# Optimization experiments

Hardware: AMD Instinct MI355X
Metric: run time of the kernel (lower is better)

The kernel has to match this reference:

```python
import jax, jax.numpy as jnp
import numpy as np

SEM_DIM = 256
AC_DIM = 36
CODEBOOK_SIZE = 8192
FSQ_LEVELS = 21
COMMIT_COST = 0.25
HALF = (FSQ_LEVELS - 1) / 2.0  # 10.0
EPS = 0.001


def setup_inputs() -> dict:
    key = jax.random.key(0)
    k1, k2 = jax.random.split(key)
    z = jax.random.normal(k1, (8, SEM_DIM + AC_DIM, 4096), dtype=jnp.float32)
    lim = 1.0 / CODEBOOK_SIZE
    codebook = jax.random.uniform(k2, (CODEBOOK_SIZE, SEM_DIM), dtype=jnp.float32,
                                  minval=-lim, maxval=lim)
    return {"z": z, "codebook": codebook}


def _round_ste(x):
    return x + jax.lax.stop_gradient(jnp.round(x) - x)


def _vq(z_sem, codebook):
    # z_sem: (B, D, T), codebook: (K, D)
    B, D, T = z_sem.shape
    z_flat = jnp.transpose(z_sem, (0, 2, 1)).reshape(B * T, D)  # (N, D)
    # pairwise squared distances via matmul: ||z||^2 - 2 z.W^T + ||W||^2
    dists = (jnp.sum(z_flat * z_flat, axis=1, keepdims=True)
             - 2.0 * jnp.matmul(z_flat, codebook.T)
             + jnp.sum(codebook * codebook, axis=1)[None, :])  # (N, K)
    indices = jnp.argmin(dists, axis=1)  # (N,)
    z_q_flat = codebook[indices]  # (N, D) gather
    z_q = jnp.transpose(z_q_flat.reshape(B, T, D), (0, 2, 1))  # (B, D, T)
    codebook_loss = jnp.mean((z_q - jax.lax.stop_gradient(z_sem)) ** 2)
    commitment_loss = COMMIT_COST * jnp.mean((jax.lax.stop_gradient(z_q) - z_sem) ** 2)
    loss = codebook_loss + commitment_loss
    z_q_ste = z_sem + jax.lax.stop_gradient(z_q - z_sem)  # straight-through
    return z_q_ste, indices.reshape(B, T), loss


def _fsq(z_ac):
    z_b = jnp.tanh(z_ac) * (HALF + EPS)
    z_q = _round_ste(z_b)
    codes = jnp.clip((z_q + HALF).astype(jnp.int32), 0, FSQ_LEVELS - 1)
    return z_q, codes


def reference(z, codebook):
    z_sem = z[:, :SEM_DIM, :]
    z_ac = z[:, SEM_DIM:, :]
    z_sem_q, sem_indices, vq_loss = _vq(z_sem, codebook)
    z_ac_q, ac_codes = _fsq(z_ac)
    z_q = jnp.concatenate([z_sem_q, z_ac_q], axis=1)
    return (z_q, sem_indices, ac_codes, vq_loss, z_ac_q)
```

## Files before the change

kernel.cpp:

```cpp
#include <hip/hip_runtime.h>
#include <math.h>

#define BB 8
#define DSEM 256
#define DAC 36
#define DTOT 292
#define TT 4096
#define NCB 8192
#define NROWS (BB*TT)

static constexpr size_t O0 = 0;
static constexpr size_t O1 = 9568256;
static constexpr size_t O2 = 9601024;
static constexpr size_t O3 = 10780672;
static constexpr size_t O4 = 10780673;

static constexpr size_t WB_AH   = 0;
static constexpr size_t WB_BH   = 16777216;
static constexpr size_t WB_TMIN = 20971520;
static constexpr size_t WB_CBT  = 37748736;
static constexpr size_t WB_RN   = 46137344;
static constexpr size_t WB_CSQ  = 46268416;
static constexpr size_t WB_LOSS = 46301184;
static constexpr size_t WB_CNT  = 46301192;
static constexpr size_t WB_RN4  = 46301200;
static constexpr size_t WB_END  = 47349776;
static constexpr unsigned WL_CAP = 4194304;

typedef _Float16 f16x8 __attribute__((ext_vector_type(8)));
typedef __attribute__((ext_vector_type(4))) float f32x4;

__device__ __forceinline__ void gload_lds16(const void* g, void* lds) {
  __builtin_amdgcn_global_load_lds(
      (const __attribute__((address_space(1))) void*)g,
      (__attribute__((address_space(3))) void*)lds, 16, 0, 0);
}


__global__ __launch_bounds__(256) void k_fsq(const float* __restrict__ z,
                                             float* __restrict__ out) {
  int e = blockIdx.x * 256 + threadIdx.x;
  int b = e / (DAC * TT);
  int rem = e - b * (DAC * TT);
  int d = rem >> 12, t = rem & 4095;
  float zv = z[((size_t)(b * DTOT + DSEM + d) << 12) + t];
  float th = (float)tanh((double)zv);
  float zb = th * 10.001f;
  float zq = rintf(zb);
  int code = (int)(zq + 10.0f);
  code = code < 0 ? 0 : (code > 20 ? 20 : code);
  out[O0 + (((size_t)(b * DTOT + DSEM + d)) << 12) + t] = zq;
  out[O2 + e] = (float)code;
  out[O4 + e] = zq;
}


__global__ __launch_bounds__(256) void k_prepB2(const float* __restrict__ cb,
                                                _Float16* __restrict__ Bh,
                                                float* __restrict__ csq,
                                                float* __restrict__ cbT4,
                                                double* __restrict__ loss,
                                                unsigned* __restrict__ counters) {
  if (blockIdx.x == 0 && threadIdx.x == 0) {
    loss[0] = 0.0; counters[0] = 0u; counters[1] = 0u;
  }
  int e = blockIdx.x * 256 + threadIdx.x;
  float4 v = reinterpret_cast<const float4*>(cb)[e];
  union { _Float16 h[4]; short4 s4; } o;
  o.h[0] = (_Float16)(v.x * -32768.0f);
  o.h[1] = (_Float16)(v.y * -32768.0f);
  o.h[2] = (_Float16)(v.z * -32768.0f);
  o.h[3] = (_Float16)(v.w * -32768.0f);
  reinterpret_cast<short4*>(Bh)[e] = o.s4;
  float s = v.x * v.x + v.y * v.y + v.z * v.z + v.w * v.w;
  for (int off = 32; off; off >>= 1) s += __shfl_xor(s, off);
  if ((threadIdx.x & 63) == 0) csq[e >> 6] = s;
  int c = e & 31, r = e >> 5;
  int u = r >> 6, k4 = r & 63;
  int j = (u << 5) + c;
  float4 w = *reinterpret_cast<const float4*>(cb + (size_t)j * 256 + k4 * 4);
  reinterpret_cast<float4*>(cbT4)[e] = w;
}

__global__ __launch_bounds__(256) void k_prepA(const float* __restrict__ z,
                                               _Float16* __restrict__ Ah,
                                               float* __restrict__ outz,
                                               double* __restrict__ rn4) {
  __shared__ float tile[64][65];
  __shared__ double rpart[4][64];
  int bid = blockIdx.x;
  int tt = bid & 63, kt = (bid >> 6) & 3, b = bid >> 8;
  int k0 = kt * 64, t0 = tt * 64;
  int tid = threadIdx.x;
  int q = tid >> 6, t2r = tid & 63;
  double acc = 0.0;
  #pragma unroll
  for (int i = 0; i < 16; ++i) {
    int kk = i * 4 + q;
    float v = z[((size_t)(b * DTOT + k0 + kk) << 12) + t0 + t2r];
    tile[t2r][kk] = v;
    acc += (double)v * (double)v;
  }
  rpart[q][t2r] = acc;
  __syncthreads();
  float* zTb = outz + (size_t)b * (DTOT * TT);
  #pragma unroll
  for (int i = 0; i < 4; ++i) {
    int flat = i * 256 + tid;
    int t2 = flat >> 4, k4g = (flat & 15) << 2;
    float f0 = tile[t2][k4g + 0], f1 = tile[t2][k4g + 1];
    float f2 = tile[t2][k4g + 2], f3 = tile[t2][k4g + 3];
    union { _Float16 h[4]; short4 s; } hh;
    hh.h[0] = (_Float16)f0; hh.h[1] = (_Float16)f1;
    hh.h[2] = (_Float16)f2; hh.h[3] = (_Float16)f3;
    *reinterpret_cast<short4*>(
        Ah + (size_t)(b * 4096 + t0 + t2) * 256 + k0 + k4g) = hh.s;
    float4 ff;
    ff.x = f0; ff.y = f1; ff.z = f2; ff.w = f3;
    *reinterpret_cast<float4*>(
        zTb + (size_t)(t0 + t2) * 256 + k0 + k4g) = ff;
  }
  if (tid < 64) {
    double s = ((rpart[0][tid] + rpart[1][tid]) + rpart[2][tid]) + rpart[3][tid];
    rn4[(size_t)kt * NROWS + (b << 12) + t0 + tid] = s;
  }
}

__global__ __launch_bounds__(256) void k_gemm(const _Float16* __restrict__ A,
                                              const _Float16* __restrict__ B,
                                              const float* __restrict__ csq,
                                              _Float16* __restrict__ tmin) {
  __shared__ char smraw[128 * 68 * 4];
  _Float16* As = (_Float16*)smraw;
  _Float16* Bs = (_Float16*)(smraw + 16384);
  float* red = (float*)smraw;
  const float SCALE = 6.103515625e-05f;

  int bid = blockIdx.x;
  int wg = (bid & 7) * 2048 + (bid >> 3);
  int mtile = wg >> 6, ntile = wg & 63;
  int rbase = mtile << 7, cbase = ntile << 7;
  int tid = threadIdx.x, lane = tid & 63, wid = tid >> 6;
  int wm = wid >> 1, wn = wid & 1;
  int l15 = lane & 15, l4 = lane >> 4;
  int sw = l15 & 7;

  f32x4 acc[4][4];
  #pragma unroll
  for (int mi = 0; mi < 4; ++mi)
    #pragma unroll
    for (int ni = 0; ni < 4; ++ni) acc[mi][ni] = (f32x4){0.f, 0.f, 0.f, 0.f};

  for (int kt = 0; kt < 4; ++kt) {
    int kb = kt << 6;
    __syncthreads();
    #pragma unroll
    for (int i = 0; i < 4; ++i) {
      int flat = (wid * 4 + i) * 64 + lane;
      int row = flat >> 3;
      int csrc = (flat & 7) ^ (row & 7);
      gload_lds16(A + (size_t)(rbase + row) * 256 + kb + (csrc << 3),
                  (char*)As + flat * 16);
      gload_lds16(B + (size_t)(cbase + row) * 256 + kb + (csrc << 3),
                  (char*)Bs + flat * 16);
    }
    __syncthreads();
    #pragma unroll
    for (int ks = 0; ks < 2; ++ks) {
      int off = ((((ks << 2) + l4) ^ sw) << 3);
      f16x8 af[4], bv[4];
      #pragma unroll
      for (int mi = 0; mi < 4; ++mi)
        af[mi] = *(const f16x8*)(As + ((wm * 64 + mi * 16 + l15) << 6) + off);
      #pragma unroll
      for (int ni = 0; ni < 4; ++ni)
        bv[ni] = *(const f16x8*)(Bs + ((wn * 64 + ni * 16 + l15) << 6) + off);
      #pragma unroll
      for (int mi = 0; mi < 4; ++mi)
        #pragma unroll
        for (int ni = 0; ni < 4; ++ni)
          acc[mi][ni] = __builtin_amdgcn_mfma_f32_16x16x32_f16(af[mi], bv[ni], acc[mi][ni], 0, 0, 0);
    }
  }

  float csv[4];
  #pragma unroll
  for (int ni = 0; ni < 4; ++ni) csv[ni] = csq[cbase + wn * 64 + ni * 16 + l15];

  __syncthreads();
  #pragma unroll
  for (int mi = 0; mi < 4; ++mi) {
    #pragma unroll
    for (int r = 0; r < 4; ++r) {
      int row = wm * 64 + mi * 16 + l4 * 4 + r;
      float v0 = fminf(fmaf(acc[mi][0][r], SCALE, csv[0]),
                       fmaf(acc[mi][1][r], SCALE, csv[1]));
      float v1 = fminf(fmaf(acc[mi][2][r], SCALE, csv[2]),
                       fmaf(acc[mi][3][r], SCALE, csv[3]));
      red[row * 68 + (wn * 2 + 0) * 16 + l15] = v0;
      red[row * 68 + (wn * 2 + 1) * 16 + l15] = v1;
    }
  }
  __syncthreads();
  if (tid < 128) {
    int row = tid;
    const float* rp = red + row * 68;
    union { _Float16 h[4]; short4 s; } uu;
    #pragma unroll
    for (int q = 0; q < 4; ++q) {
      float m = rp[q * 16];
      #pragma unroll
      for (int x = 1; x < 16; ++x) m = fminf(m, rp[q * 16 + x]);
      uu.h[q] = (_Float16)m;
    }
    *reinterpret_cast<short4*>(tmin + (size_t)(rbase + row) * 256 + ntile * 4) = uu.s;
  }
}

__global__ __launch_bounds__(256) void k_cand(const _Float16* __restrict__ tmin,
                                              const double* __restrict__ rn4,
                                              float* __restrict__ rn,
                                              unsigned* __restrict__ wl,
                                              unsigned* __restrict__ counter,
                                              unsigned long long* __restrict__ result) {
  __shared__ unsigned long long smask[16][4];
  __shared__ unsigned scnt[16];
  __shared__ unsigned soff[16];
  int tid = threadIdx.x;
  int wv = tid >> 6, lane = tid & 63;
  int row0 = blockIdx.x << 4;

  for (int rr = wv; rr < 16; rr += 4) {
    int row = row0 + rr;
    const _Float16* tp = tmin + (size_t)row * 256;
    float v[4];
    #pragma unroll
    for (int i = 0; i < 4; ++i) v[i] = (float)tp[i * 64 + lane];
    float g = fminf(fminf(v[0], v[1]), fminf(v[2], v[3]));
    #pragma unroll
    for (int off = 32; off; off >>= 1) g = fminf(g, __shfl_xor(g, off));
    float thr = g + 1.5e-4f;
    if (lane == 0) {
      result[row] = 0xFFFFFFFFFFFFFFFFULL;
      double s = ((rn4[row] + rn4[NROWS + row]) + rn4[2 * NROWS + row]) +
                 rn4[3 * NROWS + row];
      rn[row] = (float)s;
    }
    unsigned cnt = 0;
    #pragma unroll
    for (int i = 0; i < 4; ++i) {
      unsigned long long mask = __ballot(v[i] <= thr);
      if (lane == 0) smask[rr][i] = mask;
      cnt += (unsigned)__popcll(mask);
    }
    if (lane == 0) scnt[rr] = cnt;
  }
  __syncthreads();
  if (tid == 0) {
    unsigned tot = 0;
    #pragma unroll
    for (int r = 0; r < 16; ++r) { soff[r] = tot; tot += scnt[r]; }
    unsigned base = atomicAdd(counter, tot);
    #pragma unroll
    for (int r = 0; r < 16; ++r) soff[r] += base;
  }
  __syncthreads();
  for (int rr = wv; rr < 16; rr += 4) {
    int row = row0 + rr;
    unsigned off = soff[rr];
    unsigned acc = 0;
    #pragma unroll
    for (int i = 0; i < 4; ++i) {
      unsigned long long mask = smask[rr][i];
      bool c = (mask >> lane) & 1ULL;
      if (c) {
        unsigned rank = acc + (unsigned)__popcll(mask & ((1ULL << lane) - 1ULL));
        unsigned idx = off + rank;
        if (idx < WL_CAP) wl[idx] = ((unsigned)row << 8) | (unsigned)(i * 64 + lane);
      }
      acc += (unsigned)__popcll(mask);
    }
  }
}

__global__ __launch_bounds__(256) void k_scan(const float* __restrict__ zT,
                                              const float* __restrict__ cbT4,
                                              const float* __restrict__ csq,
                                              const float* __restrict__ rn,
                                              const unsigned* __restrict__ wl,
                                              const unsigned* __restrict__ counter,
                                              unsigned long long* __restrict__ result) {
  unsigned total = *counter;
  if (total > WL_CAP) total = WL_CAP;
  int tid = threadIdx.x;
  unsigned stride = gridDim.x * 8u;
  int gw = blockIdx.x * 4 + (tid >> 6);
  int half = (tid >> 5) & 1, l32 = tid & 31;
  for (unsigned it = (unsigned)(gw * 2 + half); it < total; it += stride) {
    unsigned e = wl[it];
    int row = (int)(e >> 8), u = (int)(e & 255u);
    int j = (u << 5) + l32;
    int b = row >> 12, t = row & 4095;
    const float4* zp = reinterpret_cast<const float4*>(
        zT + (size_t)b * (DTOT * TT) + (size_t)t * 256);
    const float4* cp = reinterpret_cast<const float4*>(cbT4) + ((u * 64) * 32 + l32);
    float an = rn[row], cq = csq[j];
    float m0 = 0.f, m1 = 0.f, m2 = 0.f, m3 = 0.f;
    #pragma unroll 8
    for (int k4 = 0; k4 < 64; ++k4) {
      float4 cv = cp[k4 * 32];
      float4 zv = zp[k4];
      m0 = fmaf(zv.x, cv.x, m0);
      m1 = fmaf(zv.y, cv.y, m1);
      m2 = fmaf(zv.z, cv.z, m2);
      m3 = fmaf(zv.w, cv.w, m3);
    }
    float m = (m0 + m1) + (m2 + m3);
    float d = (an - 2.f * m) + cq;
    unsigned long long pk =
        (((unsigned long long)__float_as_uint(d)) << 32) | (unsigned)j;
    #pragma unroll
    for (int off = 16; off; off >>= 1) {
      unsigned long long o = __shfl_xor(pk, off);
      if (o < pk) pk = o;
    }
    if (l32 == 0) atomicMin(result + row, pk);
  }
}

__global__ __launch_bounds__(256) void k_out(const float* __restrict__ z,
                                             const float* __restrict__ cb,
                                             const unsigned long long* __restrict__ result,
                                             float* __restrict__ out0,
                                             float* __restrict__ out1,
                                             double* __restrict__ loss,
                                             unsigned* __restrict__ done,
                                             float* __restrict__ out3) {
  __shared__ float zs[32][257];
  __shared__ float hsum[8];
  int bid = blockIdx.x;
  int tt = bid & 127, b = bid >> 7;
  int t0 = tt * 32;
  int tid = threadIdx.x;

  #pragma unroll
  for (int i = 0; i < 8; ++i) {
    int flat = i * 256 + tid;
    int d = flat >> 3, t4 = (flat & 7) * 4;
    float4 v = *reinterpret_cast<const float4*>(
        z + ((size_t)(b * DTOT + d) << 12) + t0 + t4);
    zs[t4 + 0][d] = v.x; zs[t4 + 1][d] = v.y;
    zs[t4 + 2][d] = v.z; zs[t4 + 3][d] = v.w;
  }
  __syncthreads();

  int hw = tid >> 5, l32 = tid & 31;
  float lsum = 0.f;
  #pragma unroll
  for (int p = 0; p < 4; ++p) {
    int t2 = p * 8 + hw;
    int row = (b << 12) + t0 + t2;
    unsigned j = (unsigned)(result[row] & 0xFFFFFFFFULL);
    if (l32 == 0) out1[row] = (float)j;
    const float4* cp = reinterpret_cast<const float4*>(cb + (size_t)j * 256);
    float4 c0 = cp[l32 * 2], c1 = cp[l32 * 2 + 1];
    int d0 = l32 * 8;
    float cs = 0.f, df;
    df = c0.x - zs[t2][d0 + 0]; cs = fmaf(df, df, cs); zs[t2][d0 + 0] = c0.x;
    df = c0.y - zs[t2][d0 + 1]; cs = fmaf(df, df, cs); zs[t2][d0 + 1] = c0.y;
    df = c0.z - zs[t2][d0 + 2]; cs = fmaf(df, df, cs); zs[t2][d0 + 2] = c0.z;
    df = c0.w - zs[t2][d0 + 3]; cs = fmaf(df, df, cs); zs[t2][d0 + 3] = c0.w;
    df = c1.x - zs[t2][d0 + 4]; cs = fmaf(df, df, cs); zs[t2][d0 + 4] = c1.x;
    df = c1.y - zs[t2][d0 + 5]; cs = fmaf(df, df, cs); zs[t2][d0 + 5] = c1.y;
    df = c1.z - zs[t2][d0 + 6]; cs = fmaf(df, df, cs); zs[t2][d0 + 6] = c1.z;
    df = c1.w - zs[t2][d0 + 7]; cs = fmaf(df, df, cs); zs[t2][d0 + 7] = c1.w;
    lsum += cs;
  }
  #pragma unroll
  for (int off = 16; off; off >>= 1) lsum += __shfl_xor(lsum, off);
  if (l32 == 0) hsum[hw] = lsum;
  __syncthreads();

  #pragma unroll
  for (int i = 0; i < 8; ++i) {
    int flat = i * 256 + tid;
    int d = flat >> 3, t4 = (flat & 7) * 4;
    float4 v;
    v.x = zs[t4 + 0][d]; v.y = zs[t4 + 1][d];
    v.z = zs[t4 + 2][d]; v.w = zs[t4 + 3][d];
    *reinterpret_cast<float4*>(
        out0 + ((size_t)(b * DTOT + d) << 12) + t0 + t4) = v;
  }

  if (tid == 0) {
    float tot = ((hsum[0] + hsum[1]) + (hsum[2] + hsum[3])) +
                ((hsum[4] + hsum[5]) + (hsum[6] + hsum[7]));
    atomicAdd(loss, (double)tot);
    __threadfence();
    unsigned old = atomicAdd(done, 1u);
    if (old == 1023u) {
      double total = atomicAdd(loss, 0.0);
      out3[0] = (float)(1.25 * total / 8388608.0);
    }
  }
}


__global__ __launch_bounds__(256) void k_csq(const float* __restrict__ cb,
                                             float* __restrict__ csq,
                                             double* __restrict__ loss,
                                             unsigned* __restrict__ counter) {
  if (blockIdx.x == 0 && threadIdx.x == 0) { loss[0] = 0.0; counter[0] = 0u; }
  int w = (blockIdx.x << 2) + (threadIdx.x >> 6);
  int lane = threadIdx.x & 63;
  float4 v = *reinterpret_cast<const float4*>(cb + (size_t)w * DSEM + lane * 4);
  float s = v.x * v.x + v.y * v.y + v.z * v.z + v.w * v.w;
  for (int off = 32; off; off >>= 1) s += __shfl_xor(s, off);
  if (lane == 0) csq[w] = s;
}

__global__ __launch_bounds__(256) void k_rn(const float* __restrict__ z,
                                            float* __restrict__ rn) {
  int r = blockIdx.x * 256 + threadIdx.x;
  int b = r >> 12, t = r & 4095;
  const float* p = z + ((size_t)(b * DTOT) << 12) + t;
  double acc = 0.0;
  #pragma unroll 8
  for (int d = 0; d < DSEM; ++d) {
    float v = p[(size_t)d << 12];
    acc += (double)v * (double)v;
  }
  rn[r] = (float)acc;
}

__global__ void k_fin(const double* __restrict__ loss, float* __restrict__ out3) {
  out3[0] = (float)(1.25 * loss[0] / 8388608.0);
}

__global__ __launch_bounds__(256) void k_vq(const float* __restrict__ z,
                                            const float* __restrict__ cb,
                                            const float* __restrict__ csq,
                                            const float* __restrict__ rn,
                                            float* __restrict__ pmin,
                                            int* __restrict__ pidx) {
  __shared__ float As[32][132];
  __shared__ float Bs[32][132];
  const int tid = threadIdx.x;
  const int tx = tid & 15, ty = tid >> 4;
  const int mb = blockIdx.x >> 2, s = blockIdx.x & 3;
  const int r0 = mb << 7;
  const int b = r0 >> 12, t0 = r0 & 4095;
  const int nbase = s * 2048;

  int mrow[8], jcol[8];
  #pragma unroll
  for (int i = 0; i < 4; ++i) {
    mrow[i] = ty * 4 + i;  mrow[i + 4] = 64 + ty * 4 + i;
    jcol[i] = tx * 4 + i;  jcol[i + 4] = 64 + tx * 4 + i;
  }
  float an[8];
  #pragma unroll
  for (int i = 0; i < 8; ++i) an[i] = rn[r0 + mrow[i]];

  float rmin[8]; int ridx[8];
  #pragma unroll
  for (int i = 0; i < 8; ++i) { rmin[i] = 3.402823466e38f; ridx[i] = 0; }

  for (int nc = 0; nc < 16; ++nc) {
    const int n0 = nbase + nc * 128;
    float acc[8][8];
    #pragma unroll
    for (int i = 0; i < 8; ++i)
      #pragma unroll
      for (int j = 0; j < 8; ++j) acc[i][j] = 0.f;

    for (int kc = 0; kc < 8; ++kc) {
      const int kb = kc << 5;
      __syncthreads();
      #pragma unroll
      for (int i = 0; i < 4; ++i) {
        int flat = i * 256 + tid;
        int k = flat >> 5, m4 = (flat & 31) << 2;
        float4 vv = *reinterpret_cast<const float4*>(
            z + ((size_t)(b * DTOT + kb + k) << 12) + t0 + m4);
        *reinterpret_cast<float4*>(&As[k][m4]) = vv;
      }
      #pragma unroll
      for (int i = 0; i < 4; ++i) {
        int flat = i * 256 + tid;
        int j = flat >> 3, k4 = (flat & 7) << 2;
        float4 vv = *reinterpret_cast<const float4*>(
            cb + ((size_t)(n0 + j) << 8) + kb + k4);
        Bs[k4 + 0][j] = vv.x; Bs[k4 + 1][j] = vv.y;
        Bs[k4 + 2][j] = vv.z; Bs[k4 + 3][j] = vv.w;
      }
      __syncthreads();
      #pragma unroll 8
      for (int k = 0; k < 32; ++k) {
        float a[8], bv[8];
        *reinterpret_cast<float4*>(&a[0]) = *reinterpret_cast<const float4*>(&As[k][ty * 4]);
        *reinterpret_cast<float4*>(&a[4]) = *reinterpret_cast<const float4*>(&As[k][64 + ty * 4]);
        *reinterpret_cast<float4*>(&bv[0]) = *reinterpret_cast<const float4*>(&Bs[k][tx * 4]);
        *reinterpret_cast<float4*>(&bv[4]) = *reinterpret_cast<const float4*>(&Bs[k][64 + tx * 4]);
        #pragma unroll
        for (int i = 0; i < 8; ++i)
          #pragma unroll
          for (int j = 0; j < 8; ++j) acc[i][j] = fmaf(a[i], bv[j], acc[i][j]);
      }
    }
    float cs[8];
    #pragma unroll
    for (int j = 0; j < 8; ++j) cs[j] = csq[n0 + jcol[j]];
    #pragma unroll
    for (int i = 0; i < 8; ++i) {
      #pragma unroll
      for (int j = 0; j < 8; ++j) {
        float d = (an[i] - 2.f * acc[i][j]) + cs[j];
        int jg = n0 + jcol[j];
        if (d < rmin[i] || (d == rmin[i] && jg < ridx[i])) { rmin[i] = d; ridx[i] = jg; }
      }
    }
  }
  __syncthreads();
  float* redf = &As[0][0];
  int* redi = reinterpret_cast<int*>(&Bs[0][0]);
  #pragma unroll
  for (int i = 0; i < 8; ++i) {
    redf[mrow[i] * 16 + tx] = rmin[i];
    redi[mrow[i] * 16 + tx] = ridx[i];
  }
  __syncthreads();
  if (tid < 128) {
    int row = tid;
    float bestv = redf[row * 16]; int bi = redi[row * 16];
    #pragma unroll
    for (int x = 1; x < 16; ++x) {
      float m = redf[row * 16 + x]; int ii = redi[row * 16 + x];
      if (m < bestv || (m == bestv && ii < bi)) { bestv = m; bi = ii; }
    }
    pmin[(size_t)(r0 + row) * 4 + s] = bestv;
    pidx[(size_t)(r0 + row) * 4 + s] = bi;
  }
}

__global__ __launch_bounds__(256) void k_comb(const float* __restrict__ pmin,
                                              const int* __restrict__ pidx,
                                              int* __restrict__ widx,
                                              float* __restrict__ out1) {
  int r = blockIdx.x * 256 + threadIdx.x;
  float best = pmin[r * 4]; int bi = pidx[r * 4];
  #pragma unroll
  for (int s2 = 1; s2 < 4; ++s2) {
    float m = pmin[r * 4 + s2]; int ii = pidx[r * 4 + s2];
    if (m < best || (m == best && ii < bi)) { best = m; bi = ii; }
  }
  widx[r] = bi;
  out1[r] = (float)bi;
}

__global__ __launch_bounds__(256) void k_loss_fb(const float* __restrict__ z,
                                                 const float* __restrict__ cb,
                                                 const int* __restrict__ idx,
                                                 float* __restrict__ out0,
                                                 double* __restrict__ loss) {
  float s = 0.f;
  for (int e = blockIdx.x * 256 + threadIdx.x; e < BB * DSEM * TT; e += 2048 * 256) {
    int b = e >> 20;
    int rem = e & 1048575;
    int d = rem >> 12, t = rem & 4095;
    int r = (b << 12) + t;
    int j = idx[r];
    float c = cb[(size_t)j * DSEM + d];
    size_t zi = ((size_t)(b * DTOT + d) << 12) + t;
    float zv = z[zi];
    out0[zi] = c;
    float df = c - zv;
    s += df * df;
  }
  for (int off = 32; off; off >>= 1) s += __shfl_xor(s, off);
  __shared__ float ws4[4];
  int lane = threadIdx.x & 63, w = threadIdx.x >> 6;
  if (lane == 0) ws4[w] = s;
  __syncthreads();
  if (threadIdx.x == 0) {
    float tot = ws4[0] + ws4[1] + ws4[2] + ws4[3];
    atomicAdd(loss, (double)tot);
  }
}


extern "C" void kernel_launch(void* const* d_in, const int* in_sizes, int n_in,
                              void* d_out, int out_size, void* d_ws, size_t ws_size,
                              hipStream_t stream) {
  const float* z  = (const float*)d_in[0];
  const float* cb = (const float*)d_in[1];
  float* out = (float*)d_out;

  if (ws_size >= WB_END) {
    char* wsb = (char*)d_ws;
    _Float16* Ah   = (_Float16*)(wsb + WB_AH);
    _Float16* Bh   = (_Float16*)(wsb + WB_BH);
    _Float16* tmin = (_Float16*)(wsb + WB_TMIN);
    float*    cbT4 = (float*)(wsb + WB_CBT);
    float*    rn   = (float*)(wsb + WB_RN);
    float*    csq  = (float*)(wsb + WB_CSQ);
    double*   loss = (double*)(wsb + WB_LOSS);
    unsigned* counters = (unsigned*)(wsb + WB_CNT);
    double*   rn4  = (double*)(wsb + WB_RN4);
    unsigned* wl = (unsigned*)(wsb + WB_AH);
    unsigned long long* result = (unsigned long long*)(wsb + WB_BH);
    float* zT = out + O0;

    k_prepB2<<<2048, 256, 0, stream>>>(cb, Bh, csq, cbT4, loss, counters);
    k_fsq<<<(BB * DAC * TT) / 256, 256, 0, stream>>>(z, out);
    k_prepA<<<2048, 256, 0, stream>>>(z, Ah, zT, rn4);
    k_gemm<<<16384, 256, 0, stream>>>(Ah, Bh, csq, tmin);
    k_cand<<<NROWS / 16, 256, 0, stream>>>(tmin, rn4, rn, wl, counters, result);
    k_scan<<<4096, 256, 0, stream>>>(zT, cbT4, csq, rn, wl, counters, result);
    k_out<<<1024, 256, 0, stream>>>(z, cb, result, out + O0, out + O1, loss,
                                    counters + 1, out + O3);
  } else {
    float* wsf = (float*)d_ws;
    float* csq  = wsf;
    float* rn   = wsf + 8192;
    float* pmin = wsf + 40960;
    int*   pidx = (int*)(wsf + 172032);
    int*   widx = (int*)(wsf + 303104);
    double* loss = (double*)(wsf + 335872);
    unsigned* counter = (unsigned*)(wsf + 335876);

    k_csq<<<NCB / 4, 256, 0, stream>>>(cb, csq, loss, counter);
    k_rn<<<NROWS / 256, 256, 0, stream>>>(z, rn);
    k_fsq<<<(BB * DAC * TT) / 256, 256, 0, stream>>>(z, out);
    k_vq<<<(NROWS / 128) * 4, 256, 0, stream>>>(z, cb, csq, rn, pmin, pidx);
    k_comb<<<NROWS / 256, 256, 0, stream>>>(pmin, pidx, widx, out + O1);
    k_loss_fb<<<2048, 256, 0, stream>>>(z, cb, widx, out + O0, loss);
    k_fin<<<1, 1, 0, stream>>>(loss, out + O3);
  }
}
```

Before: 366.5 us.

## Replace candidate worklist with codebook-tile-major scan using LDS-resident codebook slices

The per-tile minimum matrix is now stored transposed (tile-major), and k_cand only computes a per-row threshold instead of building a compacted worklist with atomics. k_scan is reorganised so each block owns one 32-entry codebook tile, loads that slice into shared memory once, and sweeps a quarter of the rows, ballotting candidates against the threshold and refining them with exact fp32 dot products. This removes the global atomic worklist, its capacity limit, and the repeated global reads of codebook slices. In exchange, work is less balanced: blocks whose tiles have many candidates serialise them, and every block reads the full tmin column for its rows. The tmin stores in the GEMM epilogue also become scattered 2-byte writes.

New measurement: 375.7 us. 1.03x slower.

```diff
diff --git a/kernel.cpp b/kernel.cpp
--- a/kernel.cpp
+++ b/kernel.cpp
@@ -24,8 +24,8 @@
 static constexpr size_t WB_LOSS = 46301184;
 static constexpr size_t WB_CNT  = 46301192;
 static constexpr size_t WB_RN4  = 46301200;
-static constexpr size_t WB_END  = 47349776;
-static constexpr unsigned WL_CAP = 4194304;
+static constexpr size_t WB_THR  = 47349776;
+static constexpr size_t WB_END  = 47480848;
 
 typedef _Float16 f16x8 __attribute__((ext_vector_type(8)));
 typedef __attribute__((ext_vector_type(4))) float f32x4;
@@ -129,7 +129,7 @@
 __global__ __launch_bounds__(256) void k_gemm(const _Float16* __restrict__ A,
                                               const _Float16* __restrict__ B,
                                               const float* __restrict__ csq,
-                                              _Float16* __restrict__ tmin) {
+                                              _Float16* __restrict__ tminT) {
   __shared__ char smraw[128 * 68 * 4];
   _Float16* As = (_Float16*)smraw;
   _Float16* Bs = (_Float16*)(smraw + 16384);
@@ -205,126 +205,98 @@
   if (tid < 128) {
     int row = tid;
     const float* rp = red + row * 68;
-    union { _Float16 h[4]; short4 s; } uu;
     #pragma unroll
     for (int q = 0; q < 4; ++q) {
       float m = rp[q * 16];
       #pragma unroll
       for (int x = 1; x < 16; ++x) m = fminf(m, rp[q * 16 + x]);
-      uu.h[q] = (_Float16)m;
-    }
-    *reinterpret_cast<short4*>(tmin + (size_t)(rbase + row) * 256 + ntile * 4) = uu.s;
-  }
-}
-
-__global__ __launch_bounds__(256) void k_cand(const _Float16* __restrict__ tmin,
+      tminT[(size_t)(ntile * 4 + q) * NROWS + rbase + row] = (_Float16)m;
+    }
+  }
+}
+
+__global__ __launch_bounds__(256) void k_cand(const _Float16* __restrict__ tminT,
                                               const double* __restrict__ rn4,
                                               float* __restrict__ rn,
-                                              unsigned* __restrict__ wl,
-                                              unsigned* __restrict__ counter,
+                                              float* __restrict__ rowthr,
                                               unsigned long long* __restrict__ result) {
-  __shared__ unsigned long long smask[16][4];
-  __shared__ unsigned scnt[16];
-  __shared__ unsigned soff[16];
+  __shared__ float pmin[4][64];
   int tid = threadIdx.x;
-  int wv = tid >> 6, lane = tid & 63;
-  int row0 = blockIdx.x << 4;
-
-  for (int rr = wv; rr < 16; rr += 4) {
-    int row = row0 + rr;
-    const _Float16* tp = tmin + (size_t)row * 256;
-    float v[4];
-    #pragma unroll
-    for (int i = 0; i < 4; ++i) v[i] = (float)tp[i * 64 + lane];
-    float g = fminf(fminf(v[0], v[1]), fminf(v[2], v[3]));
-    #pragma unroll
-    for (int off = 32; off; off >>= 1) g = fminf(g, __shfl_xor(g, off));
-    float thr = g + 1.5e-4f;
-    if (lane == 0) {
-      result[row] = 0xFFFFFFFFFFFFFFFFULL;
-      double s = ((rn4[row] + rn4[NROWS + row]) + rn4[2 * NROWS + row]) +
-                 rn4[3 * NROWS + row];
-      rn[row] = (float)s;
-    }
-    unsigned cnt = 0;
-    #pragma unroll
-    for (int i = 0; i < 4; ++i) {
-      unsigned long long mask = __ballot(v[i] <= thr);
-      if (lane == 0) smask[rr][i] = mask;
-      cnt += (unsigned)__popcll(mask);
-    }
-    if (lane == 0) scnt[rr] = cnt;
-  }
-  __syncthreads();
-  if (tid == 0) {
-    unsigned tot = 0;
-    #pragma unroll
-    for (int r = 0; r < 16; ++r) { soff[r] = tot; tot += scnt[r]; }
-    unsigned base = atomicAdd(counter, tot);
-    #pragma unroll
-    for (int r = 0; r < 16; ++r) soff[r] += base;
-  }
-  __syncthreads();
-  for (int rr = wv; rr < 16; rr += 4) {
-    int row = row0 + rr;
-    unsigned off = soff[rr];
-    unsigned acc = 0;
-    #pragma unroll
-    for (int i = 0; i < 4; ++i) {
-      unsigned long long mask = smask[rr][i];
-      bool c = (mask >> lane) & 1ULL;
-      if (c) {
-        unsigned rank = acc + (unsigned)__popcll(mask & ((1ULL << lane) - 1ULL));
-        unsigned idx = off + rank;
-        if (idx < WL_CAP) wl[idx] = ((unsigned)row << 8) | (unsigned)(i * 64 + lane);
-      }
-      acc += (unsigned)__popcll(mask);
-    }
+  int w = tid >> 6, lane = tid & 63;
+  int row = (blockIdx.x << 6) + lane;
+  float g = 3.402823466e38f;
+  for (int ug = 0; ug < 64; ++ug) {
+    int u = w * 64 + ug;
+    g = fminf(g, (float)tminT[(size_t)u * NROWS + row]);
+  }
+  pmin[w][lane] = g;
+  __syncthreads();
+  if (w == 0) {
+    float gg = fminf(fminf(pmin[0][lane], pmin[1][lane]),
+                     fminf(pmin[2][lane], pmin[3][lane]));
+    rowthr[row] = gg + 1.5e-4f;
+    result[row] = 0xFFFFFFFFFFFFFFFFULL;
+    double s = ((rn4[row] + rn4[NROWS + row]) + rn4[2 * NROWS + row]) +
+               rn4[3 * NROWS + row];
+    rn[row] = (float)s;
   }
 }
 
 __global__ __launch_bounds__(256) void k_scan(const float* __restrict__ zT,
-                                              const float* __restrict__ cbT4,
+                                              const float4* __restrict__ cbT4f4,
                                               const float* __restrict__ csq,
                                               const float* __restrict__ rn,
-                                              const unsigned* __restrict__ wl,
-                                              const unsigned* __restrict__ counter,
+                                              const _Float16* __restrict__ tminT,
+                                              const float* __restrict__ rowthr,
                                               unsigned long long* __restrict__ result) {
-  unsigned total = *counter;
-  if (total > WL_CAP) total = WL_CAP;
+  __shared__ float4 cbl[2048];
+  int bid = blockIdx.x;
+  int u = bid >> 2, rc = bid & 3;
   int tid = threadIdx.x;
-  unsigned stride = gridDim.x * 8u;
-  int gw = blockIdx.x * 4 + (tid >> 6);
-  int half = (tid >> 5) & 1, l32 = tid & 31;
-  for (unsigned it = (unsigned)(gw * 2 + half); it < total; it += stride) {
-    unsigned e = wl[it];
-    int row = (int)(e >> 8), u = (int)(e & 255u);
-    int j = (u << 5) + l32;
-    int b = row >> 12, t = row & 4095;
-    const float4* zp = reinterpret_cast<const float4*>(
-        zT + (size_t)b * (DTOT * TT) + (size_t)t * 256);
-    const float4* cp = reinterpret_cast<const float4*>(cbT4) + ((u * 64) * 32 + l32);
-    float an = rn[row], cq = csq[j];
-    float m0 = 0.f, m1 = 0.f, m2 = 0.f, m3 = 0.f;
-    #pragma unroll 8
-    for (int k4 = 0; k4 < 64; ++k4) {
-      float4 cv = cp[k4 * 32];
-      float4 zv = zp[k4];
-      m0 = fmaf(zv.x, cv.x, m0);
-      m1 = fmaf(zv.y, cv.y, m1);
-      m2 = fmaf(zv.z, cv.z, m2);
-      m3 = fmaf(zv.w, cv.w, m3);
-    }
-    float m = (m0 + m1) + (m2 + m3);
-    float d = (an - 2.f * m) + cq;
-    unsigned long long pk =
-        (((unsigned long long)__float_as_uint(d)) << 32) | (unsigned)j;
-    #pragma unroll
-    for (int off = 16; off; off >>= 1) {
-      unsigned long long o = __shfl_xor(pk, off);
-      if (o < pk) pk = o;
-    }
-    if (l32 == 0) atomicMin(result + row, pk);
+  #pragma unroll
+  for (int i = 0; i < 8; ++i)
+    cbl[i * 256 + tid] = cbT4f4[(size_t)u * 2048 + i * 256 + tid];
+  __syncthreads();
+  int w = tid >> 6, lane = tid & 63, l32 = tid & 31;
+  int j = (u << 5) + l32;
+  float cq = csq[j];
+  int rbase0 = rc * 8192 + w * 2048;
+  for (int chunk = 0; chunk < 32; ++chunk) {
+    int rowb = rbase0 + chunk * 64;
+    float v = (float)tminT[(size_t)u * NROWS + rowb + lane];
+    float thr = rowthr[rowb + lane];
+    unsigned long long mask = __ballot(v <= thr);
+    while (mask) {
+      int sl0 = __builtin_ctzll(mask); mask &= mask - 1;
+      int sl1 = sl0;
+      if (mask) { sl1 = __builtin_ctzll(mask); mask &= mask - 1; }
+      int sl = (lane < 32) ? sl0 : sl1;
+      int crow = rowb + sl;
+      int b = crow >> 12, t = crow & 4095;
+      const float4* zp = reinterpret_cast<const float4*>(
+          zT + (size_t)b * (DTOT * TT) + (size_t)t * 256);
+      float an = rn[crow];
+      float m0 = 0.f, m1 = 0.f, m2 = 0.f, m3 = 0.f;
+      #pragma unroll 8
+      for (int k4 = 0; k4 < 64; ++k4) {
+        float4 cv = cbl[k4 * 32 + l32];
+        float4 zv = zp[k4];
+        m0 = fmaf(zv.x, cv.x, m0);
+        m1 = fmaf(zv.y, cv.y, m1);
+        m2 = fmaf(zv.z, cv.z, m2);
+        m3 = fmaf(zv.w, cv.w, m3);
+      }
+      float m = (m0 + m1) + (m2 + m3);
+      float d = (an - 2.f * m) + cq;
+      unsigned long long pk =
+          (((unsigned long long)__float_as_uint(d)) << 32) | (unsigned)j;
+      #pragma unroll
+      for (int off = 16; off; off >>= 1) {
+        unsigned long long o = __shfl_xor(pk, off);
+        if (o < pk) pk = o;
+      }
+      if (l32 == 0) atomicMin(result + crow, pk);
+    }
   }
 }
 
@@ -598,25 +570,26 @@
 
   if (ws_size >= WB_END) {
     char* wsb = (char*)d_ws;
-    _Float16* Ah   = (_Float16*)(wsb + WB_AH);
-    _Float16* Bh   = (_Float16*)(wsb + WB_BH);
-    _Float16* tmin = (_Float16*)(wsb + WB_TMIN);
-    float*    cbT4 = (float*)(wsb + WB_CBT);
-    float*    rn   = (float*)(wsb + WB_RN);
-    float*    csq  = (float*)(wsb + WB_CSQ);
-    double*   loss = (double*)(wsb + WB_LOSS);
+    _Float16* Ah    = (_Float16*)(wsb + WB_AH);
+    _Float16* Bh    = (_Float16*)(wsb + WB_BH);
+    _Float16* tminT = (_Float16*)(wsb + WB_TMIN);
+    float*    cbT4  = (float*)(wsb + WB_CBT);
+    float*    rn    = (float*)(wsb + WB_RN);
+    float*    csq   = (float*)(wsb + WB_CSQ);
+    double*   loss  = (double*)(wsb + WB_LOSS);
     unsigned* counters = (unsigned*)(wsb + WB_CNT);
-    double*   rn4  = (double*)(wsb + WB_RN4);
-    unsigned* wl = (unsigned*)(wsb + WB_AH);
+    double*   rn4   = (double*)(wsb + WB_RN4);
+    float*    rowthr = (float*)(wsb + WB_THR);
     unsigned long long* result = (unsigned long long*)(wsb + WB_BH);
     float* zT = out + O0;
 
     k_prepB2<<<2048, 256, 0, stream>>>(cb, Bh, csq, cbT4, loss, counters);
     k_fsq<<<(BB * DAC * TT) / 256, 256, 0, stream>>>(z, out);
     k_prepA<<<2048, 256, 0, stream>>>(z, Ah, zT, rn4);
-    k_gemm<<<16384, 256, 0, stream>>>(Ah, Bh, csq, tmin);
-    k_cand<<<NROWS / 16, 256, 0, stream>>>(tmin, rn4, rn, wl, counters, result);
-    k_scan<<<4096, 256, 0, stream>>>(zT, cbT4, csq, rn, wl, counters, result);
+    k_gemm<<<16384, 256, 0, stream>>>(Ah, Bh, csq, tminT);
+    k_cand<<<NROWS / 64, 256, 0, stream>>>(tminT, rn4, rn, rowthr, result);
+    k_scan<<<1024, 256, 0, stream>>>(zT, (const float4*)cbT4, csq, rn, tminT,
+                                     rowthr, result);
     k_out<<<1024, 256, 0, stream>>>(z, cb, result, out + O0, out + O1, loss,
                                     counters + 1, out + O3);
   } else {
```
